# Optimization experiments

Hardware: AMD Instinct MI355X
Metric: run time of the kernel (lower is better)

The kernel has to match this reference:

```python
import jax, jax.numpy as jnp
import numpy as np
import math

D = 128  # hidden_dim
N_USERS = 10000
N_ITEMS = 12000
NEG_INF = -9e15


def setup_inputs() -> dict:
    key = jax.random.key(0)
    k1, k2, k3, k4, k5 = jax.random.split(key, 5)
    ufea = jax.random.normal(k1, (N_USERS, D), dtype=jnp.float32)
    inter = jax.random.normal(k2, (N_ITEMS, D), dtype=jnp.float32)
    adj = jax.random.randint(k3, (N_USERS, N_ITEMS), 0, 2, dtype=jnp.int32)
    # linear layer params (torch default init approximated with scaled normals)
    W = jax.random.normal(k4, (D, D), dtype=jnp.float32) / jnp.sqrt(jnp.float32(D))
    b = jax.random.normal(k5, (D,), dtype=jnp.float32) * 0.01
    return {"ufea": ufea, "inter": inter, "adj": adj, "W": W, "b": b}


def _leaky_relu2(x):
    # nn.LeakyReLU(2): negative_slope = 2
    return jnp.where(x > 0, x, 2.0 * x)


def reference(ufea, inter, adj, W, b):
    # GAT.forward_user with dropout in eval mode (identity).
    # Attention.forward(a=ufea, b=inter, adj)
    query = ufea @ W.T + b                      # [N, D]  nn.Linear
    scale = 1.0 / math.sqrt(D)
    scores = _leaky_relu2((query @ inter.T) * scale)   # [N, M]
    scores = jnp.where(adj > 0, scores, NEG_INF)        # mask non-edges
    attn = jax.nn.softmax(scores, axis=1)               # row softmax
    result = attn @ inter                                # [N, D]
    return result
```

## Files before the change

### kernel.cpp

```cpp
#include <hip/hip_runtime.h>
#include <cstdint>
#include <cstddef>


#define N_USERS 10000
#define N_ITEMS 12000
#define HD      128
#define QROWS   10048
#define NCHUNK  16
#define TILE    64
#define NTILES  188
#define UBLOCKS 157
#define KT_PITCH 12032

typedef __bf16 bf16x8 __attribute__((ext_vector_type(8)));
typedef __bf16 bf16x4 __attribute__((ext_vector_type(4)));
typedef __bf16 bf16x2 __attribute__((ext_vector_type(2)));
typedef float  f32x4  __attribute__((ext_vector_type(4)));
typedef int    i32x2  __attribute__((ext_vector_type(2)));

typedef const __attribute__((address_space(1))) unsigned int g_u32;
typedef __attribute__((address_space(3))) unsigned int l_u32;

__global__ __launch_bounds__(256) void cast_inter_kernel(const float* __restrict__ inter,
                                                         __bf16* __restrict__ kg,
                                                         __bf16* __restrict__ ktg) {
    __shared__ __bf16 Tl[128 * 72];
    const int t  = threadIdx.x;
    const int i0 = blockIdx.x * 64;
    for (int it = 0; it < 8; ++it) {
        int g   = it * 256 + t;
        int row = g >> 5;
        int d   = (g & 31) * 4;
        int item = i0 + row;
        if (item < N_ITEMS) {
            f32x4 v = *(const f32x4*)(inter + (size_t)item * HD + d);
            __bf16 b0 = (__bf16)v.x, b1 = (__bf16)v.y, b2 = (__bf16)v.z, b3 = (__bf16)v.w;
            bf16x4 pk = {b0, b1, b2, b3};
            *(bf16x4*)(kg + (size_t)item * HD + d) = pk;
            Tl[(d + 0) * 72 + row] = b0;
            Tl[(d + 1) * 72 + row] = b1;
            Tl[(d + 2) * 72 + row] = b2;
            Tl[(d + 3) * 72 + row] = b3;
        } else {
            Tl[(d + 0) * 72 + row] = (__bf16)0.f;
            Tl[(d + 1) * 72 + row] = (__bf16)0.f;
            Tl[(d + 2) * 72 + row] = (__bf16)0.f;
            Tl[(d + 3) * 72 + row] = (__bf16)0.f;
        }
    }
    __syncthreads();
    const int d  = t >> 1;
    const int jb = (t & 1) * 32;
    if (i0 + jb < N_ITEMS) {
        #pragma unroll
        for (int k = 0; k < 4; ++k) {
            bf16x8 v = *(const bf16x8*)&Tl[d * 72 + jb + k * 8];
            *(bf16x8*)(ktg + (size_t)d * KT_PITCH + i0 + jb + k * 8) = v;
        }
    }
}

__global__ __launch_bounds__(256) void query_kernel(const float* __restrict__ ufea,
                                                    const float* __restrict__ W,
                                                    const float* __restrict__ bias,
                                                    __bf16* __restrict__ qg) {
    const int lane = threadIdx.x & 63, wave = threadIdx.x >> 6;
    const int n = lane & 15, qd = lane >> 4;
    const int user0 = blockIdx.x * 64 + wave * 16;
    int arow = user0 + n; if (arow > N_USERS - 1) arow = N_USERS - 1;

    bf16x8 af[4];
    #pragma unroll
    for (int kk = 0; kk < 4; ++kk) {
        const float* p = ufea + (size_t)arow * HD + kk * 32 + qd * 8;
        f32x4 lo = *(const f32x4*)p, hi = *(const f32x4*)(p + 4);
        bf16x8 a;
        a[0]=(__bf16)lo.x; a[1]=(__bf16)lo.y; a[2]=(__bf16)lo.z; a[3]=(__bf16)lo.w;
        a[4]=(__bf16)hi.x; a[5]=(__bf16)hi.y; a[6]=(__bf16)hi.z; a[7]=(__bf16)hi.w;
        af[kk] = a;
    }
    #pragma unroll
    for (int nt = 0; nt < 8; ++nt) {
        f32x4 acc = {0.f, 0.f, 0.f, 0.f};
        #pragma unroll
        for (int kk = 0; kk < 4; ++kk) {
            const float* p = W + (size_t)(nt * 16 + n) * HD + kk * 32 + qd * 8;
            f32x4 lo = *(const f32x4*)p, hi = *(const f32x4*)(p + 4);
            bf16x8 b;
            b[0]=(__bf16)lo.x; b[1]=(__bf16)lo.y; b[2]=(__bf16)lo.z; b[3]=(__bf16)lo.w;
            b[4]=(__bf16)hi.x; b[5]=(__bf16)hi.y; b[6]=(__bf16)hi.z; b[7]=(__bf16)hi.w;
            acc = __builtin_amdgcn_mfma_f32_16x16x32_bf16(af[kk], b, acc, 0, 0, 0);
        }
        const float bv = bias[nt * 16 + n];
        #pragma unroll
        for (int r = 0; r < 4; ++r) {
            int row = user0 + qd * 4 + r;
            qg[(size_t)row * HD + nt * 16 + n] = (__bf16)(acc[r] + bv);
        }
    }
}

__global__ __launch_bounds__(256, 2) void fused_kernel(const __bf16* __restrict__ qg,
                                                       const __bf16* __restrict__ kg,
                                                       const __bf16* __restrict__ ktg,
                                                       const int* __restrict__ adj,
                                                       float* __restrict__ Opart,
                                                       float* __restrict__ lpart) {
    __shared__ __bf16 Kbuf[2][16 * 512];
    __shared__ __bf16 Vbuf[2][16 * 512];
    __shared__ __bf16 Pl[4][16 * 72];
    const int lane = threadIdx.x & 63, wave = threadIdx.x >> 6;
    const int n = lane & 15, qd = lane >> 4;
    const int user0 = blockIdx.y * 64 + wave * 16;
    const int chunk = blockIdx.x;
    const int t0 = (chunk * NTILES) / NCHUNK;
    const int t1 = ((chunk + 1) * NTILES) / NCHUNK;
    const float SC = (float)(1.4426950408889634 * 0.08838834764831845);

    bf16x8 qf[4];
    #pragma unroll
    for (int kk = 0; kk < 4; ++kk)
        qf[kk] = *(const bf16x8*)(qg + (size_t)(user0 + n) * HD + kk * 32 + qd * 8);

    f32x4 Oacc[8];
    #pragma unroll
    for (int dt = 0; dt < 8; ++dt) Oacc[dt] = (f32x4){0.f, 0.f, 0.f, 0.f};
    float lacc[4] = {0.f, 0.f, 0.f, 0.f};

    size_t adjOff[4];
    #pragma unroll
    for (int r = 0; r < 4; ++r) {
        int u = user0 + qd * 4 + r;
        if (u > N_USERS - 1) u = N_USERS - 1;
        adjOff[r] = (size_t)u * N_ITEMS;
    }
    __bf16* pw = &Pl[wave][0];

    auto stage = [&](int t, int b) {
        const int j0s = t * TILE;
        #pragma unroll
        for (int j = 0; j < 4; ++j) {
            const int c = wave * 4 + j;
            int row = j0s + (wave >> 1) * 32 + 2 * n + (wave & 1);
            if (row > N_ITEMS - 1) row = N_ITEMS - 1;
            const __bf16* src = kg + (size_t)row * HD + j * 32 + qd * 8;
            __builtin_amdgcn_global_load_lds((g_u32*)src, (l_u32*)(&Kbuf[b][c * 512]), 16, 0, 0);
        }
        #pragma unroll
        for (int j = 0; j < 4; ++j) {
            const int c = wave * 4 + j;
            const int dt = c >> 1, kc = c & 1;
            const __bf16* src = ktg + (size_t)(dt * 16 + n) * KT_PITCH + j0s + kc * 32 + qd * 8;
            __builtin_amdgcn_global_load_lds((g_u32*)src, (l_u32*)(&Vbuf[b][c * 512]), 16, 0, 0);
        }
    };
    auto load_adj = [&](int t, i32x2 av[2][4]) {
        #pragma unroll
        for (int h = 0; h < 2; ++h) {
            int col2 = t * TILE + h * 32 + 2 * n;
            if (col2 > N_ITEMS - 2) col2 = N_ITEMS - 2;
            #pragma unroll
            for (int r = 0; r < 4; ++r)
                av[h][r] = __builtin_nontemporal_load((const i32x2*)(adj + adjOff[r] + col2));
        }
    };

    stage(t0, 0);
    i32x2 av[2][4];
    load_adj(t0, av);

    for (int t = t0; t < t1; ++t) {
        const int cur = (t - t0) & 1;
        const int j0 = t * TILE;
        __syncthreads();

        i32x2 avn[2][4];
        if (t + 1 < t1) {
            load_adj(t + 1, avn);
            stage(t + 1, cur ^ 1);
        }

        f32x4 S[4];
        #pragma unroll
        for (int nt = 0; nt < 4; ++nt) S[nt] = (f32x4){0.f, 0.f, 0.f, 0.f};
        #pragma unroll
        for (int nt = 0; nt < 4; ++nt) {
            #pragma unroll
            for (int kk = 0; kk < 4; ++kk) {
                bf16x8 b = *(const bf16x8*)(&Kbuf[cur][(nt * 4 + kk) * 512 + lane * 8]);
                S[nt] = __builtin_amdgcn_mfma_f32_16x16x32_bf16(qf[kk], b, S[nt], 0, 0, 0);
            }
        }
        #pragma unroll
        for (int r = 0; r < 4; ++r) {
            #pragma unroll
            for (int h = 0; h < 2; ++h) {
                const int colb = j0 + h * 32 + 2 * n;
                float p01[2];
                #pragma unroll
                for (int par = 0; par < 2; ++par) {
                    const int nt = h * 2 + par;
                    float s = S[nt][r] * SC;
                    s = fminf(s, s + s);
                    const bool on = (colb + par < N_ITEMS) && (av[h][r][par] > 0);
                    float p = on ? __builtin_amdgcn_exp2f(s) : 0.f;
                    lacc[r] += p;
                    p01[par] = p;
                }
                bf16x2 pk = {(__bf16)p01[0], (__bf16)p01[1]};
                *(bf16x2*)(pw + (qd * 4 + r) * 72 + h * 32 + 2 * n) = pk;
            }
        }
        #pragma unroll
        for (int kc = 0; kc < 2; ++kc) {
            bf16x8 af = *(const bf16x8*)(pw + n * 72 + kc * 32 + qd * 8);
            #pragma unroll
            for (int dt = 0; dt < 8; ++dt) {
                bf16x8 b = *(const bf16x8*)(&Vbuf[cur][(dt * 2 + kc) * 512 + lane * 8]);
                Oacc[dt] = __builtin_amdgcn_mfma_f32_16x16x32_bf16(af, b, Oacc[dt], 0, 0, 0);
            }
        }
        #pragma unroll
        for (int h = 0; h < 2; ++h)
            #pragma unroll
            for (int r = 0; r < 4; ++r)
                av[h][r] = avn[h][r];
    }

    #pragma unroll
    for (int r = 0; r < 4; ++r) {
        float v = lacc[r];
        v += __shfl_xor(v, 1);
        v += __shfl_xor(v, 2);
        v += __shfl_xor(v, 4);
        v += __shfl_xor(v, 8);
        lacc[r] = v;
    }
    const size_t cb = (size_t)chunk * QROWS;
    #pragma unroll
    for (int r = 0; r < 4; ++r) {
        const int user = user0 + qd * 4 + r;
        if (user < N_USERS) {
            #pragma unroll
            for (int dt = 0; dt < 8; ++dt)
                Opart[(cb + user) * HD + dt * 16 + n] = Oacc[dt][r];
            if (n == 0) lpart[cb + user] = lacc[r];
        }
    }
}

__global__ __launch_bounds__(256) void combine_kernel(const float* __restrict__ Opart,
                                                      const float* __restrict__ lpart,
                                                      float* __restrict__ out) {
    const int g = blockIdx.x * 256 + threadIdx.x;
    const int base = g * 4;
    const int user = base >> 7;
    const int d = base & 127;
    f32x4 acc = {0.f, 0.f, 0.f, 0.f};
    float l = 0.f;
    #pragma unroll
    for (int c = 0; c < NCHUNK; ++c) {
        acc += *(const f32x4*)(Opart + ((size_t)c * QROWS + user) * HD + d);
        l += lpart[(size_t)c * QROWS + user];
    }
    f32x4 res = acc / l;
    *(f32x4*)(out + (size_t)user * HD + d) = res;
}

extern "C" void kernel_launch(void* const* d_in, const int* in_sizes, int n_in,
                              void* d_out, int out_size, void* d_ws, size_t ws_size,
                              hipStream_t stream) {
    const float* ufea = (const float*)d_in[0];
    const float* inter = (const float*)d_in[1];
    const int*   adj  = (const int*)d_in[2];
    const float* W    = (const float*)d_in[3];
    const float* bias = (const float*)d_in[4];
    float* out = (float*)d_out;

    char* ws = (char*)d_ws;
    __bf16* qg   = (__bf16*)(ws);
    __bf16* kg   = (__bf16*)(ws + 2572288);
    __bf16* ktg  = (__bf16*)(ws + 5644288);
    float*  Opart = (float*)(ws + 8724480);
    float*  lpart = (float*)(ws + 91037696);

    cast_inter_kernel<<<dim3(188), dim3(256), 0, stream>>>(inter, kg, ktg);
    query_kernel<<<dim3(UBLOCKS), dim3(256), 0, stream>>>(ufea, W, bias, qg);
    fused_kernel<<<dim3(NCHUNK, UBLOCKS), dim3(256), 0, stream>>>(qg, kg, ktg, adj, Opart, lpart);
    combine_kernel<<<dim3(1250), dim3(256), 0, stream>>>(Opart, lpart, out);
}
```

Measured before the change: 733.5 us.

## Pre-pack adjacency matrix into bitmask before fused attention kernel

Adds a streaming kernel that turns each group of 32 int32 adjacency entries into one 32-bit mask word. The fused attention kernel then reads mask words instead of int32 adj pairs and tests bits to decide which entries to exponentiate. The aim is to move the large adjacency read into a simple, coalesced, bandwidth-friendly pass and to cut the memory traffic and register pressure inside the MFMA loop. In exchange it adds one extra kernel launch, a workspace buffer for the mask, and still reads the full adjacency matrix once per call.

```diff
diff --git a/kernel.cpp b/kernel.cpp
--- a/kernel.cpp
+++ b/kernel.cpp
@@ -12,15 +12,34 @@
 #define NTILES  188
 #define UBLOCKS 157
 #define KT_PITCH 12032
+#define MROW    375
+#define NMASK   3750000
 
 typedef __bf16 bf16x8 __attribute__((ext_vector_type(8)));
 typedef __bf16 bf16x4 __attribute__((ext_vector_type(4)));
 typedef __bf16 bf16x2 __attribute__((ext_vector_type(2)));
 typedef float  f32x4  __attribute__((ext_vector_type(4)));
-typedef int    i32x2  __attribute__((ext_vector_type(2)));
+typedef int    i32x4  __attribute__((ext_vector_type(4)));
 
 typedef const __attribute__((address_space(1))) unsigned int g_u32;
 typedef __attribute__((address_space(3))) unsigned int l_u32;
+
+__global__ __launch_bounds__(256) void compress_adj_kernel(const int* __restrict__ adj,
+                                                           unsigned int* __restrict__ mask) {
+    const int d = blockIdx.x * 256 + threadIdx.x;
+    if (d >= NMASK) return;
+    const int* p = adj + (size_t)d * 32;
+    unsigned int m = 0;
+    #pragma unroll
+    for (int j = 0; j < 8; ++j) {
+        i32x4 v = *(const i32x4*)(p + j * 4);
+        m |= (unsigned int)(v[0] > 0) << (j * 4 + 0);
+        m |= (unsigned int)(v[1] > 0) << (j * 4 + 1);
+        m |= (unsigned int)(v[2] > 0) << (j * 4 + 2);
+        m |= (unsigned int)(v[3] > 0) << (j * 4 + 3);
+    }
+    mask[d] = m;
+}
 
 __global__ __launch_bounds__(256) void cast_inter_kernel(const float* __restrict__ inter,
                                                          __bf16* __restrict__ kg,
@@ -104,7 +123,7 @@
 __global__ __launch_bounds__(256, 2) void fused_kernel(const __bf16* __restrict__ qg,
                                                        const __bf16* __restrict__ kg,
                                                        const __bf16* __restrict__ ktg,
-                                                       const int* __restrict__ adj,
+                                                       const unsigned int* __restrict__ mask,
                                                        float* __restrict__ Opart,
                                                        float* __restrict__ lpart) {
     __shared__ __bf16 Kbuf[2][16 * 512];
@@ -128,12 +147,12 @@
     for (int dt = 0; dt < 8; ++dt) Oacc[dt] = (f32x4){0.f, 0.f, 0.f, 0.f};
     float lacc[4] = {0.f, 0.f, 0.f, 0.f};
 
-    size_t adjOff[4];
+    size_t mOff[4];
     #pragma unroll
     for (int r = 0; r < 4; ++r) {
         int u = user0 + qd * 4 + r;
         if (u > N_USERS - 1) u = N_USERS - 1;
-        adjOff[r] = (size_t)u * N_ITEMS;
+        mOff[r] = (size_t)u * MROW;
     }
     __bf16* pw = &Pl[wave][0];
 
@@ -155,29 +174,26 @@
             __builtin_amdgcn_global_load_lds((g_u32*)src, (l_u32*)(&Vbuf[b][c * 512]), 16, 0, 0);
         }
     };
-    auto load_adj = [&](int t, i32x2 av[2][4]) {
-        #pragma unroll
-        for (int h = 0; h < 2; ++h) {
-            int col2 = t * TILE + h * 32 + 2 * n;
-            if (col2 > N_ITEMS - 2) col2 = N_ITEMS - 2;
+    auto load_mask = [&](int t, unsigned int md[2][4]) {
+        #pragma unroll
+        for (int h = 0; h < 2; ++h)
             #pragma unroll
             for (int r = 0; r < 4; ++r)
-                av[h][r] = __builtin_nontemporal_load((const i32x2*)(adj + adjOff[r] + col2));
-        }
+                md[h][r] = mask[mOff[r] + t * 2 + h];
     };
 
     stage(t0, 0);
-    i32x2 av[2][4];
-    load_adj(t0, av);
+    unsigned int md[2][4];
+    load_mask(t0, md);
 
     for (int t = t0; t < t1; ++t) {
         const int cur = (t - t0) & 1;
         const int j0 = t * TILE;
         __syncthreads();
 
-        i32x2 avn[2][4];
+        unsigned int mdn[2][4];
         if (t + 1 < t1) {
-            load_adj(t + 1, avn);
+            load_mask(t + 1, mdn);
             stage(t + 1, cur ^ 1);
         }
 
@@ -203,7 +219,7 @@
                     const int nt = h * 2 + par;
                     float s = S[nt][r] * SC;
                     s = fminf(s, s + s);
-                    const bool on = (colb + par < N_ITEMS) && (av[h][r][par] > 0);
+                    const bool on = (colb + par < N_ITEMS) && ((md[h][r] >> (2 * n + par)) & 1u);
                     float p = on ? __builtin_amdgcn_exp2f(s) : 0.f;
                     lacc[r] += p;
                     p01[par] = p;
@@ -225,7 +241,7 @@
         for (int h = 0; h < 2; ++h)
             #pragma unroll
             for (int r = 0; r < 4; ++r)
-                av[h][r] = avn[h][r];
+                md[h][r] = mdn[h][r];
     }
 
     #pragma unroll
@@ -279,14 +295,16 @@
     float* out = (float*)d_out;
 
     char* ws = (char*)d_ws;
-    __bf16* qg   = (__bf16*)(ws);
-    __bf16* kg   = (__bf16*)(ws + 2572288);
-    __bf16* ktg  = (__bf16*)(ws + 5644288);
-    float*  Opart = (float*)(ws + 8724480);
-    float*  lpart = (float*)(ws + 91037696);
-
+    __bf16*       qg   = (__bf16*)(ws);
+    __bf16*       kg   = (__bf16*)(ws + 2572288);
+    __bf16*       ktg  = (__bf16*)(ws + 5644288);
+    unsigned int* mb   = (unsigned int*)(ws + 8724480);
+    float*        Opart = (float*)(ws + 23726080);
+    float*        lpart = (float*)(ws + 106039296);
+
+    compress_adj_kernel<<<dim3(14649), dim3(256), 0, stream>>>(adj, mb);
     cast_inter_kernel<<<dim3(188), dim3(256), 0, stream>>>(inter, kg, ktg);
     query_kernel<<<dim3(UBLOCKS), dim3(256), 0, stream>>>(ufea, W, bias, qg);
-    fused_kernel<<<dim3(NCHUNK, UBLOCKS), dim3(256), 0, stream>>>(qg, kg, ktg, adj, Opart, lpart);
+    fused_kernel<<<dim3(NCHUNK, UBLOCKS), dim3(256), 0, stream>>>(qg, kg, ktg, mb, Opart, lpart);
     combine_kernel<<<dim3(1250), dim3(256), 0, stream>>>(Opart, lpart, out);
 }
```

New measurement: 811.0 us. 1.11x slower.

## Process 32 users per wave to reuse K/V tiles and drop double buffering

Applied to the files above, without the earlier changes.

Each wave now handles two 16-user groups (128 users per block), so every K and V fragment read from LDS feeds two MFMAs. The item permutation changes so each lane covers 4 consecutive columns, which lets adj be read as 16-byte vectors. The double-buffered prefetch pipeline is replaced by a single buffer with load-then-sync each tile, which frees LDS but exposes load latency. Grid height halves, workspace offsets and the combine bounds are adjusted to match the padded row count.

```diff
diff --git a/kernel.cpp b/kernel.cpp
--- a/kernel.cpp
+++ b/kernel.cpp
@@ -6,18 +6,19 @@
 #define N_USERS 10000
 #define N_ITEMS 12000
 #define HD      128
-#define QROWS   10048
+#define QROWS   10112
 #define NCHUNK  16
 #define TILE    64
 #define NTILES  188
-#define UBLOCKS 157
+#define UBLOCKS 79
+#define QBLOCKS 158
 #define KT_PITCH 12032
 
 typedef __bf16 bf16x8 __attribute__((ext_vector_type(8)));
 typedef __bf16 bf16x4 __attribute__((ext_vector_type(4)));
 typedef __bf16 bf16x2 __attribute__((ext_vector_type(2)));
 typedef float  f32x4  __attribute__((ext_vector_type(4)));
-typedef int    i32x2  __attribute__((ext_vector_type(2)));
+typedef int    i32x4  __attribute__((ext_vector_type(4)));
 
 typedef const __attribute__((address_space(1))) unsigned int g_u32;
 typedef __attribute__((address_space(3))) unsigned int l_u32;
@@ -52,12 +53,10 @@
     __syncthreads();
     const int d  = t >> 1;
     const int jb = (t & 1) * 32;
-    if (i0 + jb < N_ITEMS) {
-        #pragma unroll
-        for (int k = 0; k < 4; ++k) {
-            bf16x8 v = *(const bf16x8*)&Tl[d * 72 + jb + k * 8];
-            *(bf16x8*)(ktg + (size_t)d * KT_PITCH + i0 + jb + k * 8) = v;
-        }
+    #pragma unroll
+    for (int k = 0; k < 4; ++k) {
+        bf16x8 v = *(const bf16x8*)&Tl[d * 72 + jb + k * 8];
+        *(bf16x8*)(ktg + (size_t)d * KT_PITCH + i0 + jb + k * 8) = v;
     }
 }
 
@@ -107,147 +106,141 @@
                                                        const int* __restrict__ adj,
                                                        float* __restrict__ Opart,
                                                        float* __restrict__ lpart) {
-    __shared__ __bf16 Kbuf[2][16 * 512];
-    __shared__ __bf16 Vbuf[2][16 * 512];
-    __shared__ __bf16 Pl[4][16 * 72];
+    __shared__ __bf16 Kbuf[16 * 512];
+    __shared__ __bf16 Vbuf[16 * 512];
+    __shared__ __bf16 Pl[4][32 * 72];
     const int lane = threadIdx.x & 63, wave = threadIdx.x >> 6;
     const int n = lane & 15, qd = lane >> 4;
-    const int user0 = blockIdx.y * 64 + wave * 16;
+    const int user0 = blockIdx.y * 128 + wave * 32;
     const int chunk = blockIdx.x;
     const int t0 = (chunk * NTILES) / NCHUNK;
     const int t1 = ((chunk + 1) * NTILES) / NCHUNK;
     const float SC = (float)(1.4426950408889634 * 0.08838834764831845);
 
-    bf16x8 qf[4];
-    #pragma unroll
-    for (int kk = 0; kk < 4; ++kk)
-        qf[kk] = *(const bf16x8*)(qg + (size_t)(user0 + n) * HD + kk * 32 + qd * 8);
-
-    f32x4 Oacc[8];
-    #pragma unroll
-    for (int dt = 0; dt < 8; ++dt) Oacc[dt] = (f32x4){0.f, 0.f, 0.f, 0.f};
-    float lacc[4] = {0.f, 0.f, 0.f, 0.f};
-
-    size_t adjOff[4];
-    #pragma unroll
-    for (int r = 0; r < 4; ++r) {
-        int u = user0 + qd * 4 + r;
-        if (u > N_USERS - 1) u = N_USERS - 1;
-        adjOff[r] = (size_t)u * N_ITEMS;
-    }
+    bf16x8 qf[2][4];
+    #pragma unroll
+    for (int g = 0; g < 2; ++g)
+        #pragma unroll
+        for (int kk = 0; kk < 4; ++kk)
+            qf[g][kk] = *(const bf16x8*)(qg + (size_t)(user0 + g * 16 + n) * HD + kk * 32 + qd * 8);
+
+    f32x4 Oacc[2][8];
+    #pragma unroll
+    for (int g = 0; g < 2; ++g)
+        #pragma unroll
+        for (int dt = 0; dt < 8; ++dt) Oacc[g][dt] = (f32x4){0.f, 0.f, 0.f, 0.f};
+    float lacc[2][4] = {{0.f,0.f,0.f,0.f},{0.f,0.f,0.f,0.f}};
+
+    int adjOff[2][4];
+    #pragma unroll
+    for (int g = 0; g < 2; ++g)
+        #pragma unroll
+        for (int r = 0; r < 4; ++r) {
+            int u = user0 + g * 16 + qd * 4 + r;
+            if (u > N_USERS - 1) u = N_USERS - 1;
+            adjOff[g][r] = u * N_ITEMS;
+        }
     __bf16* pw = &Pl[wave][0];
 
-    auto stage = [&](int t, int b) {
-        const int j0s = t * TILE;
+    for (int t = t0; t < t1; ++t) {
+        const int j0 = t * TILE;
+        __syncthreads();
+
         #pragma unroll
         for (int j = 0; j < 4; ++j) {
             const int c = wave * 4 + j;
-            int row = j0s + (wave >> 1) * 32 + 2 * n + (wave & 1);
+            int row = j0 + 4 * n + wave;
             if (row > N_ITEMS - 1) row = N_ITEMS - 1;
             const __bf16* src = kg + (size_t)row * HD + j * 32 + qd * 8;
-            __builtin_amdgcn_global_load_lds((g_u32*)src, (l_u32*)(&Kbuf[b][c * 512]), 16, 0, 0);
+            __builtin_amdgcn_global_load_lds((g_u32*)src, (l_u32*)(&Kbuf[c * 512]), 16, 0, 0);
         }
         #pragma unroll
         for (int j = 0; j < 4; ++j) {
             const int c = wave * 4 + j;
             const int dt = c >> 1, kc = c & 1;
-            const __bf16* src = ktg + (size_t)(dt * 16 + n) * KT_PITCH + j0s + kc * 32 + qd * 8;
-            __builtin_amdgcn_global_load_lds((g_u32*)src, (l_u32*)(&Vbuf[b][c * 512]), 16, 0, 0);
-        }
-    };
-    auto load_adj = [&](int t, i32x2 av[2][4]) {
-        #pragma unroll
-        for (int h = 0; h < 2; ++h) {
-            int col2 = t * TILE + h * 32 + 2 * n;
-            if (col2 > N_ITEMS - 2) col2 = N_ITEMS - 2;
-            #pragma unroll
-            for (int r = 0; r < 4; ++r)
-                av[h][r] = __builtin_nontemporal_load((const i32x2*)(adj + adjOff[r] + col2));
-        }
-    };
-
-    stage(t0, 0);
-    i32x2 av[2][4];
-    load_adj(t0, av);
-
-    for (int t = t0; t < t1; ++t) {
-        const int cur = (t - t0) & 1;
-        const int j0 = t * TILE;
+            const __bf16* src = ktg + (size_t)(dt * 16 + n) * KT_PITCH + j0 + kc * 32 + qd * 8;
+            __builtin_amdgcn_global_load_lds((g_u32*)src, (l_u32*)(&Vbuf[c * 512]), 16, 0, 0);
+        }
+        i32x4 av[2][4];
+        {
+            int col4 = j0 + 4 * n;
+            if (col4 > N_ITEMS - 4) col4 = N_ITEMS - 4;
+            #pragma unroll
+            for (int g = 0; g < 2; ++g)
+                #pragma unroll
+                for (int r = 0; r < 4; ++r)
+                    av[g][r] = __builtin_nontemporal_load((const i32x4*)(adj + adjOff[g][r] + col4));
+        }
         __syncthreads();
 
-        i32x2 avn[2][4];
-        if (t + 1 < t1) {
-            load_adj(t + 1, avn);
-            stage(t + 1, cur ^ 1);
-        }
-
-        f32x4 S[4];
-        #pragma unroll
-        for (int nt = 0; nt < 4; ++nt) S[nt] = (f32x4){0.f, 0.f, 0.f, 0.f};
+        f32x4 S[2][4];
+        #pragma unroll
+        for (int g = 0; g < 2; ++g)
+            #pragma unroll
+            for (int nt = 0; nt < 4; ++nt) S[g][nt] = (f32x4){0.f, 0.f, 0.f, 0.f};
         #pragma unroll
         for (int nt = 0; nt < 4; ++nt) {
             #pragma unroll
             for (int kk = 0; kk < 4; ++kk) {
-                bf16x8 b = *(const bf16x8*)(&Kbuf[cur][(nt * 4 + kk) * 512 + lane * 8]);
-                S[nt] = __builtin_amdgcn_mfma_f32_16x16x32_bf16(qf[kk], b, S[nt], 0, 0, 0);
-            }
-        }
-        #pragma unroll
-        for (int r = 0; r < 4; ++r) {
-            #pragma unroll
-            for (int h = 0; h < 2; ++h) {
-                const int colb = j0 + h * 32 + 2 * n;
-                float p01[2];
+                bf16x8 b = *(const bf16x8*)(&Kbuf[(nt * 4 + kk) * 512 + lane * 8]);
+                S[0][nt] = __builtin_amdgcn_mfma_f32_16x16x32_bf16(qf[0][kk], b, S[0][nt], 0, 0, 0);
+                S[1][nt] = __builtin_amdgcn_mfma_f32_16x16x32_bf16(qf[1][kk], b, S[1][nt], 0, 0, 0);
+            }
+        }
+        #pragma unroll
+        for (int g = 0; g < 2; ++g) {
+            #pragma unroll
+            for (int r = 0; r < 4; ++r) {
+                bf16x4 pk;
                 #pragma unroll
-                for (int par = 0; par < 2; ++par) {
-                    const int nt = h * 2 + par;
-                    float s = S[nt][r] * SC;
+                for (int nt = 0; nt < 4; ++nt) {
+                    float s = S[g][nt][r] * SC;
                     s = fminf(s, s + s);
-                    const bool on = (colb + par < N_ITEMS) && (av[h][r][par] > 0);
+                    const bool on = (j0 + 4 * n + nt < N_ITEMS) && (av[g][r][nt] > 0);
                     float p = on ? __builtin_amdgcn_exp2f(s) : 0.f;
-                    lacc[r] += p;
-                    p01[par] = p;
+                    lacc[g][r] += p;
+                    pk[nt] = (__bf16)p;
                 }
-                bf16x2 pk = {(__bf16)p01[0], (__bf16)p01[1]};
-                *(bf16x2*)(pw + (qd * 4 + r) * 72 + h * 32 + 2 * n) = pk;
+                *(bf16x4*)(pw + (g * 16 + qd * 4 + r) * 72 + 4 * n) = pk;
             }
         }
         #pragma unroll
         for (int kc = 0; kc < 2; ++kc) {
-            bf16x8 af = *(const bf16x8*)(pw + n * 72 + kc * 32 + qd * 8);
+            bf16x8 af0 = *(const bf16x8*)(pw + (0 * 16 + n) * 72 + kc * 32 + qd * 8);
+            bf16x8 af1 = *(const bf16x8*)(pw + (1 * 16 + n) * 72 + kc * 32 + qd * 8);
             #pragma unroll
             for (int dt = 0; dt < 8; ++dt) {
-                bf16x8 b = *(const bf16x8*)(&Vbuf[cur][(dt * 2 + kc) * 512 + lane * 8]);
-                Oacc[dt] = __builtin_amdgcn_mfma_f32_16x16x32_bf16(af, b, Oacc[dt], 0, 0, 0);
-            }
-        }
-        #pragma unroll
-        for (int h = 0; h < 2; ++h)
-            #pragma unroll
-            for (int r = 0; r < 4; ++r)
-                av[h][r] = avn[h][r];
-    }
-
-    #pragma unroll
-    for (int r = 0; r < 4; ++r) {
-        float v = lacc[r];
-        v += __shfl_xor(v, 1);
-        v += __shfl_xor(v, 2);
-        v += __shfl_xor(v, 4);
-        v += __shfl_xor(v, 8);
-        lacc[r] = v;
-    }
+                bf16x8 b = *(const bf16x8*)(&Vbuf[(dt * 2 + kc) * 512 + lane * 8]);
+                Oacc[0][dt] = __builtin_amdgcn_mfma_f32_16x16x32_bf16(af0, b, Oacc[0][dt], 0, 0, 0);
+                Oacc[1][dt] = __builtin_amdgcn_mfma_f32_16x16x32_bf16(af1, b, Oacc[1][dt], 0, 0, 0);
+            }
+        }
+    }
+
+    #pragma unroll
+    for (int g = 0; g < 2; ++g)
+        #pragma unroll
+        for (int r = 0; r < 4; ++r) {
+            float v = lacc[g][r];
+            v += __shfl_xor(v, 1);
+            v += __shfl_xor(v, 2);
+            v += __shfl_xor(v, 4);
+            v += __shfl_xor(v, 8);
+            lacc[g][r] = v;
+        }
     const size_t cb = (size_t)chunk * QROWS;
     #pragma unroll
-    for (int r = 0; r < 4; ++r) {
-        const int user = user0 + qd * 4 + r;
-        if (user < N_USERS) {
-            #pragma unroll
-            for (int dt = 0; dt < 8; ++dt)
-                Opart[(cb + user) * HD + dt * 16 + n] = Oacc[dt][r];
-            if (n == 0) lpart[cb + user] = lacc[r];
-        }
-    }
+    for (int g = 0; g < 2; ++g)
+        #pragma unroll
+        for (int r = 0; r < 4; ++r) {
+            const int user = user0 + g * 16 + qd * 4 + r;
+            if (user < N_USERS) {
+                #pragma unroll
+                for (int dt = 0; dt < 8; ++dt)
+                    Opart[(cb + user) * HD + dt * 16 + n] = Oacc[g][dt][r];
+                if (n == 0) lpart[cb + user] = lacc[g][r];
+            }
+        }
 }
 
 __global__ __launch_bounds__(256) void combine_kernel(const float* __restrict__ Opart,
@@ -264,8 +257,10 @@
         acc += *(const f32x4*)(Opart + ((size_t)c * QROWS + user) * HD + d);
         l += lpart[(size_t)c * QROWS + user];
     }
-    f32x4 res = acc / l;
-    *(f32x4*)(out + (size_t)user * HD + d) = res;
+    if (user < N_USERS) {
+        f32x4 res = acc / l;
+        *(f32x4*)(out + (size_t)user * HD + d) = res;
+    }
 }
 
 extern "C" void kernel_launch(void* const* d_in, const int* in_sizes, int n_in,
@@ -280,13 +275,13 @@
 
     char* ws = (char*)d_ws;
     __bf16* qg   = (__bf16*)(ws);
-    __bf16* kg   = (__bf16*)(ws + 2572288);
-    __bf16* ktg  = (__bf16*)(ws + 5644288);
-    float*  Opart = (float*)(ws + 8724480);
-    float*  lpart = (float*)(ws + 91037696);
+    __bf16* kg   = (__bf16*)(ws + 2588672);
+    __bf16* ktg  = (__bf16*)(ws + 5660672);
+    float*  Opart = (float*)(ws + 8740864);
+    float*  lpart = (float*)(ws + 91578368);
 
     cast_inter_kernel<<<dim3(188), dim3(256), 0, stream>>>(inter, kg, ktg);
-    query_kernel<<<dim3(UBLOCKS), dim3(256), 0, stream>>>(ufea, W, bias, qg);
+    query_kernel<<<dim3(QBLOCKS), dim3(256), 0, stream>>>(ufea, W, bias, qg);
     fused_kernel<<<dim3(NCHUNK, UBLOCKS), dim3(256), 0, stream>>>(qg, kg, ktg, adj, Opart, lpart);
-    combine_kernel<<<dim3(1250), dim3(256), 0, stream>>>(Opart, lpart, out);
-}
+    combine_kernel<<<dim3(1264), dim3(256), 0, stream>>>(Opart, lpart, out);
+}
```

After: 687.8 us. -6.2%, faster.
